# Kernel optimization log

Hardware: AMD Instinct MI355X
Metric: run time of the kernel (lower is better)

## Reference

```python
import jax, jax.numpy as jnp
import numpy as np

D_MODEL, H, D_K, D_V, D_FF = 1024, 16, 64, 64, 4096
B, L = 2, 2048
EPS = 1e-5


def layer_norm(x, g, b):
    mu = jnp.mean(x, axis=-1, keepdims=True)
    var = jnp.mean(jnp.square(x - mu), axis=-1, keepdims=True)
    return (x - mu) * jax.lax.rsqrt(var + EPS) * g + b


def setup_inputs() -> dict:
    key = jax.random.key(0)
    ks = jax.random.split(key, 12)
    s = 0.02
    x = jax.random.normal(ks[0], (B, L, D_MODEL), dtype=jnp.float32)
    Wq = jax.random.normal(ks[1], (H, D_MODEL, D_K), dtype=jnp.float32) * s
    Wk = jax.random.normal(ks[2], (H, D_MODEL, D_K), dtype=jnp.float32) * s
    Wv = jax.random.normal(ks[3], (H, D_MODEL, D_V), dtype=jnp.float32) * s
    bq = jnp.zeros((H, D_K), dtype=jnp.float32)
    bk = jnp.zeros((H, D_K), dtype=jnp.float32)
    bv = jnp.zeros((H, D_V), dtype=jnp.float32)
    Wo = jax.random.normal(ks[4], (H * D_V, D_MODEL), dtype=jnp.float32) * s
    W1 = jax.random.normal(ks[5], (D_MODEL, D_FF), dtype=jnp.float32) * s
    b1 = jnp.zeros((D_FF,), dtype=jnp.float32)
    W2 = jax.random.normal(ks[6], (D_FF, D_MODEL), dtype=jnp.float32) * s
    ln1_g = jnp.ones((D_MODEL,), dtype=jnp.float32)
    ln1_b = jnp.zeros((D_MODEL,), dtype=jnp.float32)
    ln2_g = jnp.ones((D_MODEL,), dtype=jnp.float32)
    ln2_b = jnp.zeros((D_MODEL,), dtype=jnp.float32)
    return dict(x=x, Wq=Wq, bq=bq, Wk=Wk, bk=bk, Wv=Wv, bv=bv, Wo=Wo,
                ln1_g=ln1_g, ln1_b=ln1_b, W1=W1, b1=b1, W2=W2,
                ln2_g=ln2_g, ln2_b=ln2_b)


def reference(x, Wq, bq, Wk, bk, Wv, bv, Wo, ln1_g, ln1_b, W1, b1, W2, ln2_g, ln2_b):
    # Batched multi-head attention (all heads at once, equivalent to the
    # per-head Python loop in the original module).
    Q = jnp.einsum('bld,hdk->bhlk', x, Wq) + bq[None, :, None, :]
    K = jnp.einsum('bld,hdk->bhlk', x, Wk) + bk[None, :, None, :]
    V = jnp.einsum('bld,hdv->bhlv', x, Wv) + bv[None, :, None, :]
    scores = jnp.einsum('bhlk,bhmk->bhlm', Q, K) * (1.0 / jnp.sqrt(jnp.float32(D_K)))
    attn = jax.nn.softmax(scores, axis=-1)
    O = jnp.einsum('bhlm,bhmv->bhlv', attn, V)        # [b,h,l,dv]
    O = jnp.transpose(O, (0, 2, 1, 3)).reshape(x.shape[0], x.shape[1], H * D_V)
    mha = O @ Wo                                       # [b,l,d_model]
    # residual + LayerNorm (dropout_prob=0 -> identity)
    h1 = layer_norm(x + mha, ln1_g, ln1_b)
    ff = jax.nn.relu(h1 @ W1 + b1) @ W2
    return layer_norm(h1 + ff, ln2_g, ln2_b)
```

## Files before the change

kernel.cpp:

```cpp
#include <hip/hip_runtime.h>

typedef unsigned short u16;
typedef unsigned int u32;
typedef short bf16x8 __attribute__((ext_vector_type(8)));
typedef float f32x4 __attribute__((ext_vector_type(4)));
typedef unsigned int u32x2 __attribute__((ext_vector_type(2)));
typedef unsigned int u32x4 __attribute__((ext_vector_type(4)));

#define D_MODEL 1024
#define NH 16
#define DK 64
#define DFF 4096
#define BATCH 2
#define SEQ 2048
#define BL (BATCH*SEQ)
#define NQKV 3072
#define Q_SCALE 0.18033688011f

__device__ __forceinline__ float bfraw2f(u16 u) {
    union { u32 i; float f; } c; c.i = ((u32)u) << 16; return c.f;
}
__device__ __forceinline__ u16 f2bfraw(float f) {
    union { float f; u32 i; } c; c.f = f;
    u32 i = c.i;
    u32 lsb = (i >> 16) & 1u;
    i += 0x7fffu + lsb;
    return (u16)(i >> 16);
}
__device__ __forceinline__ u32 fasu(float f) {
    union { float f; u32 i; } c; c.f = f; return c.i;
}
__device__ __forceinline__ u32 pack_bf2(float lo, float hi) {
    return __builtin_amdgcn_perm(fasu(hi) + 0x8000u, fasu(lo) + 0x8000u,
                                 0x07060302u);
}
__device__ __forceinline__ void gload_lds16(const u16* g, u16* l) {
    __builtin_amdgcn_global_load_lds(
        (const __attribute__((address_space(1))) void*)g,
        (__attribute__((address_space(3))) void*)l, 16, 0, 0);
}

__global__ __launch_bounds__(256) void cast_f32_bf16(const float* __restrict__ in,
                                                     u16* __restrict__ out) {
    int i = (blockIdx.x * 256 + threadIdx.x) * 4;
    f32x4 v = *(const f32x4*)&in[i];
#pragma unroll
    for (int j = 0; j < 4; j++) out[i + j] = f2bfraw(v[j]);
}


__global__ __launch_bounds__(256) void transpose2d(const float* __restrict__ in,
                                                   u16* __restrict__ out,
                                                   int R, int C) {
    __shared__ u16 t[64][65];
    int c0 = blockIdx.x * 64, r0 = blockIdx.y * 64;
    int col = threadIdx.x & 63, rr = threadIdx.x >> 6;
    for (int i = rr; i < 64; i += 4)
        t[i][col] = f2bfraw(in[(size_t)(r0 + i) * C + c0 + col]);
    __syncthreads();
    for (int i = rr; i < 64; i += 4)
        out[(size_t)(c0 + i) * R + r0 + col] = t[col][i];
}

__global__ __launch_bounds__(256) void transpose_wqkv(const float* __restrict__ Wq,
                                                      const float* __restrict__ Wk,
                                                      const float* __restrict__ Wv,
                                                      u16* __restrict__ out) {
    __shared__ u16 t[64][65];
    int d0 = blockIdx.x * 64;
    int h = blockIdx.y;
    int ms = blockIdx.z;
    const float* W = (ms == 0) ? Wq : (ms == 1) ? Wk : Wv;
    const float* src = W + (size_t)h * D_MODEL * DK;
    int col = threadIdx.x & 63, rr = threadIdx.x >> 6;
    for (int i = rr; i < 64; i += 4)
        t[i][col] = f2bfraw(src[(size_t)(d0 + i) * DK + col]);
    __syncthreads();
    u16* dst = out + (size_t)(ms * 1024 + h * 64) * D_MODEL;
    for (int i = rr; i < 64; i += 4)
        dst[(size_t)i * D_MODEL + d0 + col] = t[col][i];
}

__global__ __launch_bounds__(256) void concat_bias(const float* __restrict__ bq,
                                                   const float* __restrict__ bk,
                                                   const float* __restrict__ bv,
                                                   float* __restrict__ out) {
    int i = blockIdx.x * 256 + threadIdx.x;
    out[i] = (i < 1024) ? bq[i] : (i < 2048) ? bk[i - 1024] : bv[i - 2048];
}


template <int OUT_F32, int RELU, int HASBIAS, int SPLITK, int SCALEQ, int VSTORE>
__global__ __launch_bounds__(256, 4) void gemm_bt(const u16* __restrict__ A,
                                                  const u16* __restrict__ Bt,
                                                  const float* __restrict__ bias,
                                                  void* __restrict__ Cout,
                                                  u16* __restrict__ vtout,
                                                  int M, int N, int K) {
    __shared__ __attribute__((aligned(16))) u16 As[128 * 64];
    __shared__ __attribute__((aligned(16))) u16 Bs[128 * 64];
    const int tid = threadIdx.x;
    const int lane = tid & 63, wid = tid >> 6;
    const int quad = lane >> 4, l16 = lane & 15;
    const int m0 = blockIdx.x * 128, n0 = blockIdx.y * 128;
    const int z = (SPLITK > 1) ? blockIdx.z : 0;
    const int Klen = K / SPLITK;
    const int kend = (z + 1) * Klen;
    const int wm = (wid >> 1) * 64, wn = (wid & 1) * 64;

    f32x4 acc[4][4];
#pragma unroll
    for (int i = 0; i < 4; i++)
#pragma unroll
        for (int j = 0; j < 4; j++) acc[i][j] = (f32x4){0.f, 0.f, 0.f, 0.f};

    const int srow = lane >> 3, scol = (lane & 7) * 8;

    for (int kb = z * Klen; kb < kend; kb += 64) {
#pragma unroll
        for (int p = 0; p < 4; p++) {
            int c = wid * 4 + p;
            int row = c * 8 + srow;
            gload_lds16(&A[(size_t)(m0 + row) * K + kb + scol], &As[c * 512]);
            gload_lds16(&Bt[(size_t)(n0 + row) * K + kb + scol], &Bs[c * 512]);
        }
        __syncthreads();
#pragma unroll
        for (int kh = 0; kh < 2; kh++) {
            bf16x8 af[4], bf[4];
#pragma unroll
            for (int t = 0; t < 4; t++) {
                af[t] = *(const bf16x8*)&As[(wm + t * 16 + l16) * 64 + kh * 32 + quad * 8];
                bf[t] = *(const bf16x8*)&Bs[(wn + t * 16 + l16) * 64 + kh * 32 + quad * 8];
            }
#pragma unroll
            for (int i = 0; i < 4; i++)
#pragma unroll
                for (int j = 0; j < 4; j++)
                    acc[i][j] = __builtin_amdgcn_mfma_f32_16x16x32_bf16(
                        af[i], bf[j], acc[i][j], 0, 0, 0);
        }
        __syncthreads();
    }

    if (VSTORE && n0 >= 2048) {
#pragma unroll
        for (int i = 0; i < 4; i++) {
            int row0 = m0 + wm + i * 16 + quad * 4;
            int bb = row0 >> 11, l = row0 & 2047;
#pragma unroll
            for (int j = 0; j < 4; j++) {
                int col = n0 + wn + j * 16 + l16;
                float bv = HASBIAS ? bias[col] : 0.f;
                int dv = col - 2048;
                u32x2 w;
                w.x = pack_bf2(acc[i][j][0] + bv, acc[i][j][1] + bv);
                w.y = pack_bf2(acc[i][j][2] + bv, acc[i][j][3] + bv);
                *(u32x2*)&vtout[((size_t)(bb * 1024 + dv)) * 2048 + l] = w;
            }
        }
        return;
    }

    float* outf = (float*)Cout + (size_t)z * M * N;
#pragma unroll
    for (int i = 0; i < 4; i++) {
#pragma unroll
        for (int j = 0; j < 4; j++) {
#pragma unroll
            for (int r = 0; r < 4; r++) {
                int row = m0 + wm + i * 16 + quad * 4 + r;
                int col = n0 + wn + j * 16 + l16;
                float v = acc[i][j][r];
                if (HASBIAS) v += bias[col];
                if (RELU) v = v > 0.f ? v : 0.f;
                if (SCALEQ && col < 1024) v *= Q_SCALE;
                if (OUT_F32)
                    outf[(size_t)row * N + col] = v;
                else
                    ((u16*)Cout)[(size_t)row * N + col] = f2bfraw(v);
            }
        }
    }
}

__global__ __launch_bounds__(512, 4) void attn_kernel(const u16* __restrict__ qkv,
                                                      const u16* __restrict__ vt,
                                                      u16* __restrict__ O) {
    __shared__ __attribute__((aligned(16))) u16 Ks[2][128 * 64];
    __shared__ __attribute__((aligned(16))) u16 Vs[64 * 128];

    const int tid = threadIdx.x;
    const int lane = tid & 63, wid = tid >> 6;
    const int quad = lane >> 4, l16 = lane & 15;
    const int sw = l16 & 7;
    const int b = blockIdx.z, h = blockIdx.y;
    const int q0 = blockIdx.x * 128 + wid * 16;

    const size_t qrow = (size_t)(b * SEQ + q0 + l16) * NQKV + h * DK;
    const bf16x8 qf0 = *(const bf16x8*)&qkv[qrow + quad * 8];
    const bf16x8 qf1 = *(const bf16x8*)&qkv[qrow + 32 + quad * 8];

    const u16* Kbase = qkv + (size_t)(b * SEQ) * NQKV + D_MODEL + h * DK;
    const u16* Vbase = vt + (size_t)((b * NH + h) * DK) * SEQ;

    f32x4 oacc[4];
#pragma unroll
    for (int d = 0; d < 4; d++) oacc[d] = (f32x4){0.f, 0.f, 0.f, 0.f};
    float lr = 0.f;
    const f32x4 Z = {0.f, 0.f, 0.f, 0.f};

    auto stage_k = [&](int kt2, int buf) {
#pragma unroll
        for (int p = 0; p < 2; p++) {
            int seg = p * 8 + wid;
            int row = seg * 8 + (lane >> 3);
            int chunk = (lane & 7) ^ (lane >> 3);
            gload_lds16(&Kbase[(size_t)(kt2 + row) * NQKV + chunk * 8],
                        &Ks[buf][seg * 512]);
        }
    };
    bf16x8 vreg[2];
    auto load_v = [&](int kt2) {
#pragma unroll
        for (int p = 0; p < 2; p++) {
            int s = p * 512 + tid;
            vreg[p] = *(const bf16x8*)&Vbase[(size_t)(s >> 4) * SEQ + kt2 + (s & 15) * 8];
        }
    };
    stage_k(0, 0);
    load_v(0);

    for (int t = 0; t < SEQ / 128; t++) {
        const int kt = t * 128;
#pragma unroll
        for (int p = 0; p < 2; p++) {
            int s = p * 512 + tid;
            int vr = s >> 4, vc = s & 15;
            int chunkA = (vc >> 2) * 4 + (vc & 1) * 2;
            int rem = ((vc >> 1) & 1) * 4;
            u32x4 kv = __builtin_bit_cast(u32x4, vreg[p]);
            *(u32x2*)&Vs[vr * 128 + ((chunkA ^ (vr & 7)) * 8) + rem] =
                (u32x2){kv.x, kv.y};
            *(u32x2*)&Vs[vr * 128 + (((chunkA + 1) ^ (vr & 7)) * 8) + rem] =
                (u32x2){kv.z, kv.w};
        }
        __syncthreads();

        if (t + 1 < SEQ / 128) {
            stage_k(kt + 128, (t + 1) & 1);
            load_v(kt + 128);
        }

        const u16* kb = Ks[t & 1];

        f32x4 sacc[8];
        __builtin_amdgcn_s_setprio(1);
#pragma unroll
        for (int nt = 0; nt < 8; nt++) {
            const u16* krow = &kb[(nt * 16 + l16) * 64];
            bf16x8 kf0 = *(const bf16x8*)&krow[(quad ^ sw) * 8];
            bf16x8 kf1 = *(const bf16x8*)&krow[((4 + quad) ^ sw) * 8];
            f32x4 s0 = __builtin_amdgcn_mfma_f32_16x16x32_bf16(kf0, qf0, Z, 0, 0, 0);
            sacc[nt] = __builtin_amdgcn_mfma_f32_16x16x32_bf16(kf1, qf1, s0, 0, 0, 0);
        }
        __builtin_amdgcn_s_setprio(0);

        u32 wreg[8][2];
#pragma unroll
        for (int nt = 0; nt < 8; nt++) {
            float p0 = __builtin_amdgcn_exp2f(sacc[nt][0]);
            float p1 = __builtin_amdgcn_exp2f(sacc[nt][1]);
            float p2 = __builtin_amdgcn_exp2f(sacc[nt][2]);
            float p3 = __builtin_amdgcn_exp2f(sacc[nt][3]);
            lr += (p0 + p1) + (p2 + p3);
            wreg[nt][0] = pack_bf2(p0, p1);
            wreg[nt][1] = pack_bf2(p2, p3);
        }

        __builtin_amdgcn_s_setprio(1);
#pragma unroll
        for (int ks = 0; ks < 4; ks++) {
            u32x4 pw = (u32x4){wreg[2 * ks][0], wreg[2 * ks][1],
                               wreg[2 * ks + 1][0], wreg[2 * ks + 1][1]};
            bf16x8 pf = __builtin_bit_cast(bf16x8, pw);
#pragma unroll
            for (int d = 0; d < 4; d++) {
                bf16x8 vf = *(const bf16x8*)&Vs[(d * 16 + l16) * 128 +
                                                (((ks * 4 + quad) ^ sw) * 8)];
                oacc[d] = __builtin_amdgcn_mfma_f32_16x16x32_bf16(vf, pf, oacc[d], 0, 0, 0);
            }
        }
        __builtin_amdgcn_s_setprio(0);
        __syncthreads();
    }

    lr += __shfl_xor(lr, 16, 64);
    lr += __shfl_xor(lr, 32, 64);
    float iv = 1.f / lr;

    size_t row = (size_t)(b * SEQ + q0 + l16);
#pragma unroll
    for (int d = 0; d < 4; d++) {
        float o0 = oacc[d][0] * iv, o1 = oacc[d][1] * iv;
        float o2 = oacc[d][2] * iv, o3 = oacc[d][3] * iv;
        u32x2 w;
        w.x = ((u32)f2bfraw(o1) << 16) | f2bfraw(o0);
        w.y = ((u32)f2bfraw(o3) << 16) | f2bfraw(o2);
        *(u32x2*)&O[row * D_MODEL + h * DK + d * 16 + quad * 4] = w;
    }
}

__global__ __launch_bounds__(256) void ln3_kernel(const float* __restrict__ xa,
                                                  const float* __restrict__ xb,
                                                  const float* __restrict__ xc,
                                                  const float* __restrict__ g,
                                                  const float* __restrict__ be,
                                                  u16* __restrict__ out_bf,
                                                  float* __restrict__ out_f) {
    int row = blockIdx.x;
    int tid = threadIdx.x;
    const float* pa = xa + (size_t)row * D_MODEL;
    const float* pb = xb + (size_t)row * D_MODEL;
    const float* pc = xc + (size_t)row * D_MODEL;
    int c = tid * 4;
    f32x4 av = *(const f32x4*)&pa[c];
    f32x4 bv = *(const f32x4*)&pb[c];
    f32x4 cv = *(const f32x4*)&pc[c];
    float v[4];
    float s = 0.f, ss = 0.f;
#pragma unroll
    for (int i = 0; i < 4; i++) {
        v[i] = av[i] + bv[i] + cv[i];
        s += v[i];
        ss += v[i] * v[i];
    }
#pragma unroll
    for (int off = 32; off; off >>= 1) {
        s += __shfl_down(s, off, 64);
        ss += __shfl_down(ss, off, 64);
    }
    __shared__ float red[8];
    int wid = tid >> 6, lane = tid & 63;
    if (lane == 0) { red[wid] = s; red[4 + wid] = ss; }
    __syncthreads();
    if (tid == 0) {
        red[0] = red[0] + red[1] + red[2] + red[3];
        red[4] = red[4] + red[5] + red[6] + red[7];
    }
    __syncthreads();
    float mu = red[0] * (1.f / D_MODEL);
    float var = red[4] * (1.f / D_MODEL) - mu * mu;
    float rs = rsqrtf(var + 1e-5f);
#pragma unroll
    for (int i = 0; i < 4; i++) {
        float o = (v[i] - mu) * rs * g[c + i] + be[c + i];
        if (out_f) out_f[(size_t)row * D_MODEL + c + i] = o;
        if (out_bf) out_bf[(size_t)row * D_MODEL + c + i] = f2bfraw(o);
    }
}

extern "C" void kernel_launch(void* const* d_in, const int* in_sizes, int n_in,
                              void* d_out, int out_size, void* d_ws, size_t ws_size,
                              hipStream_t stream) {
    const float* x   = (const float*)d_in[0];
    const float* Wq  = (const float*)d_in[1];
    const float* bq  = (const float*)d_in[2];
    const float* Wk  = (const float*)d_in[3];
    const float* bk  = (const float*)d_in[4];
    const float* Wv  = (const float*)d_in[5];
    const float* bv  = (const float*)d_in[6];
    const float* Wo  = (const float*)d_in[7];
    const float* g1  = (const float*)d_in[8];
    const float* be1 = (const float*)d_in[9];
    const float* W1  = (const float*)d_in[10];
    const float* b1  = (const float*)d_in[11];
    const float* W2  = (const float*)d_in[12];
    const float* g2  = (const float*)d_in[13];
    const float* be2 = (const float*)d_in[14];

    char* w = (char*)d_ws;
    auto alloc = [&](size_t bytes) {
        char* p = w;
        w += (bytes + 255) & ~(size_t)255;
        return p;
    };
    u16* wqkv_t = (u16*)alloc((size_t)NQKV * D_MODEL * 2);
    u16* wo_t   = (u16*)alloc((size_t)D_MODEL * D_MODEL * 2);
    u16* w1_t   = (u16*)alloc((size_t)DFF * D_MODEL * 2);
    u16* w2_t   = (u16*)alloc((size_t)D_MODEL * DFF * 2);
    float* bqkv = (float*)alloc((size_t)NQKV * 4);
    u16* x_bf   = (u16*)alloc((size_t)BL * D_MODEL * 2);
    u16* qkvbuf = (u16*)alloc((size_t)BL * NQKV * 2);
    u16* vtbuf  = (u16*)alloc((size_t)BATCH * NH * DK * SEQ * 2);
    u16* obuf   = (u16*)alloc((size_t)BL * D_MODEL * 2);
    float* mha_p = (float*)alloc((size_t)2 * BL * D_MODEL * 4);
    u16* h1_bf  = (u16*)alloc((size_t)BL * D_MODEL * 2);
    float* h1_f = (float*)alloc((size_t)BL * D_MODEL * 4);
    u16* ffa    = (u16*)alloc((size_t)BL * DFF * 2);
    float* ffb_p = (float*)alloc((size_t)2 * BL * D_MODEL * 4);

    cast_f32_bf16<<<dim3(BL * D_MODEL / 1024), 256, 0, stream>>>(x, x_bf);
    transpose_wqkv<<<dim3(16, 16, 3), 256, 0, stream>>>(Wq, Wk, Wv, wqkv_t);
    transpose2d<<<dim3(16, 16), 256, 0, stream>>>(Wo, wo_t, 1024, 1024);
    transpose2d<<<dim3(64, 16), 256, 0, stream>>>(W1, w1_t, 1024, 4096);
    transpose2d<<<dim3(16, 64), 256, 0, stream>>>(W2, w2_t, 4096, 1024);
    concat_bias<<<dim3(12), 256, 0, stream>>>(bq, bk, bv, bqkv);

    gemm_bt<0, 0, 1, 1, 1, 1><<<dim3(32, 24), 256, 0, stream>>>(
        x_bf, wqkv_t, bqkv, qkvbuf, vtbuf, BL, NQKV, D_MODEL);
    attn_kernel<<<dim3(16, 16, 2), 512, 0, stream>>>(qkvbuf, vtbuf, obuf);
    gemm_bt<1, 0, 0, 2, 0, 0><<<dim3(32, 8, 2), 256, 0, stream>>>(
        obuf, wo_t, nullptr, mha_p, nullptr, BL, D_MODEL, D_MODEL);
    ln3_kernel<<<dim3(BL), 256, 0, stream>>>(x, mha_p, mha_p + (size_t)BL * D_MODEL,
                                             g1, be1, h1_bf, h1_f);
    gemm_bt<0, 1, 1, 1, 0, 0><<<dim3(32, 32), 256, 0, stream>>>(
        h1_bf, w1_t, b1, ffa, nullptr, BL, DFF, D_MODEL);
    gemm_bt<1, 0, 0, 2, 0, 0><<<dim3(32, 8, 2), 256, 0, stream>>>(
        ffa, w2_t, nullptr, ffb_p, nullptr, BL, D_MODEL, DFF);
    ln3_kernel<<<dim3(BL), 256, 0, stream>>>(h1_f, ffb_p, ffb_p + (size_t)BL * D_MODEL,
                                             g2, be2, nullptr, (float*)d_out);
}
```

Baseline: 369.7 us.

## Replace GEMM with larger-tile double-buffered swizzled kernel

Replaces the 128x128 GEMM with a 512-thread kernel using 256-wide N tiles (BM 256 or 128). It double-buffers LDS loads so the next K tile is fetched while the current one computes, and XOR-swizzles LDS layout to avoid bank conflicts. It also remaps workgroup order across XCDs and raises wave priority around MFMA. Larger tiles cut global traffic per FLOP but reduce block count, which may underfill CUs for some GEMMs.

```diff
diff --git a/kernel.cpp b/kernel.cpp
--- a/kernel.cpp
+++ b/kernel.cpp
@@ -90,67 +90,99 @@
 }
 
 
-template <int OUT_F32, int RELU, int HASBIAS, int SPLITK, int SCALEQ, int VSTORE>
-__global__ __launch_bounds__(256, 4) void gemm_bt(const u16* __restrict__ A,
-                                                  const u16* __restrict__ Bt,
-                                                  const float* __restrict__ bias,
-                                                  void* __restrict__ Cout,
-                                                  u16* __restrict__ vtout,
-                                                  int M, int N, int K) {
-    __shared__ __attribute__((aligned(16))) u16 As[128 * 64];
-    __shared__ __attribute__((aligned(16))) u16 Bs[128 * 64];
+template <int BM, int OUT_F32, int RELU, int HASBIAS, int SPLITK, int SCALEQ, int VSTORE>
+__global__ __launch_bounds__(512, 2) void gemm2(const u16* __restrict__ A,
+                                                const u16* __restrict__ Bt,
+                                                const float* __restrict__ bias,
+                                                void* __restrict__ Cout,
+                                                u16* __restrict__ vtout,
+                                                int M, int N, int K) {
+    constexpr int MF = BM / 32;
+    __shared__ __attribute__((aligned(16))) u16 As[2][BM * 64];
+    __shared__ __attribute__((aligned(16))) u16 Bs[2][256 * 64];
     const int tid = threadIdx.x;
     const int lane = tid & 63, wid = tid >> 6;
     const int quad = lane >> 4, l16 = lane & 15;
-    const int m0 = blockIdx.x * 128, n0 = blockIdx.y * 128;
+
+    int nwg = gridDim.x * gridDim.y;
+    int flat = blockIdx.y * gridDim.x + blockIdx.x;
+    if ((nwg & 7) == 0) {
+        int q = nwg >> 3;
+        flat = (flat & 7) * q + (flat >> 3);
+    }
+    const int m0 = (flat % gridDim.x) * BM;
+    const int n0 = (flat / gridDim.x) * 256;
+
     const int z = (SPLITK > 1) ? blockIdx.z : 0;
     const int Klen = K / SPLITK;
-    const int kend = (z + 1) * Klen;
-    const int wm = (wid >> 1) * 64, wn = (wid & 1) * 64;
-
-    f32x4 acc[4][4];
-#pragma unroll
-    for (int i = 0; i < 4; i++)
+    const int NT = Klen / 64;
+    const int kb0 = z * Klen;
+
+    const int wrow = (wid >> 2) * (BM / 2);
+    const int wcol = (wid & 3) * 64;
+
+    f32x4 acc[MF][4];
+#pragma unroll
+    for (int i = 0; i < MF; i++)
 #pragma unroll
         for (int j = 0; j < 4; j++) acc[i][j] = (f32x4){0.f, 0.f, 0.f, 0.f};
 
-    const int srow = lane >> 3, scol = (lane & 7) * 8;
-
-    for (int kb = z * Klen; kb < kend; kb += 64) {
+    auto stage = [&](int kb, int slot) {
+#pragma unroll
+        for (int p = 0; p < BM / 64; p++) {
+            int ew = p * 512 + wid * 64;
+            int e = ew + lane;
+            int row = e >> 3, ch = e & 7;
+            gload_lds16(&A[(size_t)(m0 + row) * K + kb + ((ch ^ (row & 7)) * 8)],
+                        &As[slot][ew * 8]);
+        }
 #pragma unroll
         for (int p = 0; p < 4; p++) {
-            int c = wid * 4 + p;
-            int row = c * 8 + srow;
-            gload_lds16(&A[(size_t)(m0 + row) * K + kb + scol], &As[c * 512]);
-            gload_lds16(&Bt[(size_t)(n0 + row) * K + kb + scol], &Bs[c * 512]);
-        }
+            int ew = p * 512 + wid * 64;
+            int e = ew + lane;
+            int row = e >> 3, ch = e & 7;
+            gload_lds16(&Bt[(size_t)(n0 + row) * K + kb + ((ch ^ (row & 7)) * 8)],
+                        &Bs[slot][ew * 8]);
+        }
+    };
+
+    stage(kb0, 0);
+    for (int t = 0; t < NT; t++) {
         __syncthreads();
-#pragma unroll
-        for (int kh = 0; kh < 2; kh++) {
-            bf16x8 af[4], bf[4];
-#pragma unroll
-            for (int t = 0; t < 4; t++) {
-                af[t] = *(const bf16x8*)&As[(wm + t * 16 + l16) * 64 + kh * 32 + quad * 8];
-                bf[t] = *(const bf16x8*)&Bs[(wn + t * 16 + l16) * 64 + kh * 32 + quad * 8];
+        if (t + 1 < NT) stage(kb0 + (t + 1) * 64, (t + 1) & 1);
+        const u16* as = As[t & 1];
+        const u16* bs = Bs[t & 1];
+        __builtin_amdgcn_s_setprio(1);
+        bf16x8 bfr[4][2];
+#pragma unroll
+        for (int j = 0; j < 4; j++) {
+            int rb = wcol + j * 16 + l16;
+#pragma unroll
+            for (int kh = 0; kh < 2; kh++)
+                bfr[j][kh] = *(const bf16x8*)&bs[rb * 64 + (((kh * 4 + quad) ^ (rb & 7)) * 8)];
+        }
+#pragma unroll
+        for (int i = 0; i < MF; i++) {
+            int ra = wrow + i * 16 + l16;
+            bf16x8 a0 = *(const bf16x8*)&as[ra * 64 + ((quad ^ (ra & 7)) * 8)];
+            bf16x8 a1 = *(const bf16x8*)&as[ra * 64 + (((4 + quad) ^ (ra & 7)) * 8)];
+#pragma unroll
+            for (int j = 0; j < 4; j++) {
+                acc[i][j] = __builtin_amdgcn_mfma_f32_16x16x32_bf16(a0, bfr[j][0], acc[i][j], 0, 0, 0);
+                acc[i][j] = __builtin_amdgcn_mfma_f32_16x16x32_bf16(a1, bfr[j][1], acc[i][j], 0, 0, 0);
             }
-#pragma unroll
-            for (int i = 0; i < 4; i++)
-#pragma unroll
-                for (int j = 0; j < 4; j++)
-                    acc[i][j] = __builtin_amdgcn_mfma_f32_16x16x32_bf16(
-                        af[i], bf[j], acc[i][j], 0, 0, 0);
-        }
-        __syncthreads();
+        }
+        __builtin_amdgcn_s_setprio(0);
     }
 
     if (VSTORE && n0 >= 2048) {
 #pragma unroll
-        for (int i = 0; i < 4; i++) {
-            int row0 = m0 + wm + i * 16 + quad * 4;
+        for (int i = 0; i < MF; i++) {
+            int row0 = m0 + wrow + i * 16 + quad * 4;
             int bb = row0 >> 11, l = row0 & 2047;
 #pragma unroll
             for (int j = 0; j < 4; j++) {
-                int col = n0 + wn + j * 16 + l16;
+                int col = n0 + wcol + j * 16 + l16;
                 float bv = HASBIAS ? bias[col] : 0.f;
                 int dv = col - 2048;
                 u32x2 w;
@@ -164,13 +196,13 @@
 
     float* outf = (float*)Cout + (size_t)z * M * N;
 #pragma unroll
-    for (int i = 0; i < 4; i++) {
+    for (int i = 0; i < MF; i++) {
 #pragma unroll
         for (int j = 0; j < 4; j++) {
 #pragma unroll
             for (int r = 0; r < 4; r++) {
-                int row = m0 + wm + i * 16 + quad * 4 + r;
-                int col = n0 + wn + j * 16 + l16;
+                int row = m0 + wrow + i * 16 + quad * 4 + r;
+                int col = n0 + wcol + j * 16 + l16;
                 float v = acc[i][j][r];
                 if (HASBIAS) v += bias[col];
                 if (RELU) v = v > 0.f ? v : 0.f;
@@ -407,16 +439,16 @@
     transpose2d<<<dim3(16, 64), 256, 0, stream>>>(W2, w2_t, 4096, 1024);
     concat_bias<<<dim3(12), 256, 0, stream>>>(bq, bk, bv, bqkv);
 
-    gemm_bt<0, 0, 1, 1, 1, 1><<<dim3(32, 24), 256, 0, stream>>>(
+    gemm2<256, 0, 0, 1, 1, 1, 1><<<dim3(16, 12), 512, 0, stream>>>(
         x_bf, wqkv_t, bqkv, qkvbuf, vtbuf, BL, NQKV, D_MODEL);
     attn_kernel<<<dim3(16, 16, 2), 512, 0, stream>>>(qkvbuf, vtbuf, obuf);
-    gemm_bt<1, 0, 0, 2, 0, 0><<<dim3(32, 8, 2), 256, 0, stream>>>(
+    gemm2<128, 1, 0, 0, 2, 0, 0><<<dim3(32, 4, 2), 512, 0, stream>>>(
         obuf, wo_t, nullptr, mha_p, nullptr, BL, D_MODEL, D_MODEL);
     ln3_kernel<<<dim3(BL), 256, 0, stream>>>(x, mha_p, mha_p + (size_t)BL * D_MODEL,
                                              g1, be1, h1_bf, h1_f);
-    gemm_bt<0, 1, 1, 1, 0, 0><<<dim3(32, 32), 256, 0, stream>>>(
+    gemm2<256, 0, 1, 1, 1, 0, 0><<<dim3(16, 16), 512, 0, stream>>>(
         h1_bf, w1_t, b1, ffa, nullptr, BL, DFF, D_MODEL);
-    gemm_bt<1, 0, 0, 2, 0, 0><<<dim3(32, 8, 2), 256, 0, stream>>>(
+    gemm2<128, 1, 0, 0, 2, 0, 0><<<dim3(32, 4, 2), 512, 0, stream>>>(
         ffa, w2_t, nullptr, ffb_p, nullptr, BL, D_MODEL, DFF);
     ln3_kernel<<<dim3(BL), 256, 0, stream>>>(h1_f, ffb_p, ffb_p + (size_t)BL * D_MODEL,
                                              g2, be2, nullptr, (float*)d_out);
```

Result: no change. 376.9 us (+2.0%).

## Add 256x256 pipelined GEMM kernel for QKV and FFN1 projections

Applied to the files above, without the earlier changes.

Introduces a new GEMM kernel with 256x256 tiles and 512 threads. It double-buffers swizzled LDS stages loaded directly from global memory, interleaves loads with MFMA phases under barriers and priority hints, and remaps workgroups for L2 locality. The kernel replaces the 128x128 gemm_bt for the QKV projection (with the V-transpose epilogue moved over) and for the first FFN GEMM. This aims to raise data reuse per tile and hide load latency. The trade-off is fewer workgroups (192 and 256) on a GPU with many CUs, plus more register pressure.

```diff
diff --git a/kernel.cpp b/kernel.cpp
--- a/kernel.cpp
+++ b/kernel.cpp
@@ -89,7 +89,6 @@
     out[i] = (i < 1024) ? bq[i] : (i < 2048) ? bk[i - 1024] : bv[i - 2048];
 }
 
-
 template <int OUT_F32, int RELU, int HASBIAS, int SPLITK, int SCALEQ, int VSTORE>
 __global__ __launch_bounds__(256, 4) void gemm_bt(const u16* __restrict__ A,
                                                   const u16* __restrict__ Bt,
@@ -143,25 +142,6 @@
         __syncthreads();
     }
 
-    if (VSTORE && n0 >= 2048) {
-#pragma unroll
-        for (int i = 0; i < 4; i++) {
-            int row0 = m0 + wm + i * 16 + quad * 4;
-            int bb = row0 >> 11, l = row0 & 2047;
-#pragma unroll
-            for (int j = 0; j < 4; j++) {
-                int col = n0 + wn + j * 16 + l16;
-                float bv = HASBIAS ? bias[col] : 0.f;
-                int dv = col - 2048;
-                u32x2 w;
-                w.x = pack_bf2(acc[i][j][0] + bv, acc[i][j][1] + bv);
-                w.y = pack_bf2(acc[i][j][2] + bv, acc[i][j][3] + bv);
-                *(u32x2*)&vtout[((size_t)(bb * 1024 + dv)) * 2048 + l] = w;
-            }
-        }
-        return;
-    }
-
     float* outf = (float*)Cout + (size_t)z * M * N;
 #pragma unroll
     for (int i = 0; i < 4; i++) {
@@ -171,6 +151,194 @@
             for (int r = 0; r < 4; r++) {
                 int row = m0 + wm + i * 16 + quad * 4 + r;
                 int col = n0 + wn + j * 16 + l16;
+                float v = acc[i][j][r];
+                if (HASBIAS) v += bias[col];
+                if (RELU) v = v > 0.f ? v : 0.f;
+                if (SCALEQ && col < 1024) v *= Q_SCALE;
+                if (OUT_F32)
+                    outf[(size_t)row * N + col] = v;
+                else
+                    ((u16*)Cout)[(size_t)row * N + col] = f2bfraw(v);
+            }
+        }
+    }
+}
+
+template <int OUT_F32, int RELU, int HASBIAS, int SCALEQ, int VSTORE>
+__global__ __launch_bounds__(512, 2) void gemm5(const u16* __restrict__ A,
+                                                const u16* __restrict__ Bt,
+                                                const float* __restrict__ bias,
+                                                void* __restrict__ Cout,
+                                                u16* __restrict__ vtout,
+                                                int M, int N, int K) {
+    __shared__ __attribute__((aligned(16))) u16 As[2][2][256 * 32];
+    __shared__ __attribute__((aligned(16))) u16 Bs[2][2][256 * 32];
+    const int tid = threadIdx.x;
+    const int lane = tid & 63, wid = tid >> 6;
+    const int quad = lane >> 4, l16 = lane & 15;
+
+    int nwg = gridDim.x * gridDim.y;
+    int flat = blockIdx.y * gridDim.x + blockIdx.x;
+    if ((nwg & 7) == 0) {
+        int q = nwg >> 3;
+        flat = (flat & 7) * q + (flat >> 3);
+    }
+    const int m0 = (flat % gridDim.x) * 256;
+    const int n0 = (flat / gridDim.x) * 256;
+
+    const int NTt = K >> 6;
+    const int wrow = (wid >> 2) * 128;
+    const int wcol = (wid & 3) * 64;
+
+    f32x4 acc[8][4];
+#pragma unroll
+    for (int i = 0; i < 8; i++)
+#pragma unroll
+        for (int j = 0; j < 4; j++) acc[i][j] = (f32x4){0.f, 0.f, 0.f, 0.f};
+
+    auto stageA = [&](int w, int kh) {
+        if (w >= NTt) return;
+        u16* dst = As[w & 1][kh];
+#pragma unroll
+        for (int p = 0; p < 2; p++) {
+            int e = p * 512 + tid;
+            int row = e >> 2, ch = e & 3;
+            gload_lds16(&A[(size_t)(m0 + row) * K + (w << 6) + (kh << 5) +
+                           (((ch ^ (row & 3))) << 3)],
+                        &dst[e * 8]);
+        }
+    };
+    auto stageB = [&](int w, int kh) {
+        if (w >= NTt) return;
+        u16* dst = Bs[w & 1][kh];
+#pragma unroll
+        for (int p = 0; p < 2; p++) {
+            int e = p * 512 + tid;
+            int row = e >> 2, ch = e & 3;
+            gload_lds16(&Bt[(size_t)(n0 + row) * K + (w << 6) + (kh << 5) +
+                            (((ch ^ (row & 3))) << 3)],
+                        &dst[e * 8]);
+        }
+    };
+
+    stageA(0, 0); stageB(0, 0);
+    stageA(0, 1); stageB(0, 1);
+    stageA(1, 0); stageB(1, 0);
+    asm volatile("s_waitcnt vmcnt(4)" ::: "memory");
+    __builtin_amdgcn_s_barrier();
+
+    for (int w = 0; w < NTt; w++) {
+        const u16* as0 = As[w & 1][0];
+        const u16* as1 = As[w & 1][1];
+        const u16* bs0 = Bs[w & 1][0];
+        const u16* bs1 = Bs[w & 1][1];
+        bf16x8 af[8], bf0, bf1;
+
+#pragma unroll
+        for (int i = 0; i < 8; i++) {
+            int ra = wrow + i * 16 + l16;
+            af[i] = *(const bf16x8*)&as0[ra * 32 + ((quad ^ (ra & 3)) * 8)];
+        }
+        {
+            int rb0 = wcol + l16, rb1 = wcol + 16 + l16;
+            bf0 = *(const bf16x8*)&bs0[rb0 * 32 + ((quad ^ (rb0 & 3)) * 8)];
+            bf1 = *(const bf16x8*)&bs0[rb1 * 32 + ((quad ^ (rb1 & 3)) * 8)];
+        }
+        stageA(w + 1, 1);
+        __builtin_amdgcn_s_barrier();
+        __builtin_amdgcn_s_setprio(1);
+#pragma unroll
+        for (int i = 0; i < 8; i++) {
+            acc[i][0] = __builtin_amdgcn_mfma_f32_16x16x32_bf16(af[i], bf0, acc[i][0], 0, 0, 0);
+            acc[i][1] = __builtin_amdgcn_mfma_f32_16x16x32_bf16(af[i], bf1, acc[i][1], 0, 0, 0);
+        }
+        __builtin_amdgcn_s_setprio(0);
+        __builtin_amdgcn_s_barrier();
+
+        {
+            int rb2 = wcol + 32 + l16, rb3 = wcol + 48 + l16;
+            bf0 = *(const bf16x8*)&bs0[rb2 * 32 + ((quad ^ (rb2 & 3)) * 8)];
+            bf1 = *(const bf16x8*)&bs0[rb3 * 32 + ((quad ^ (rb3 & 3)) * 8)];
+        }
+        stageB(w + 1, 1);
+        __builtin_amdgcn_s_barrier();
+        __builtin_amdgcn_s_setprio(1);
+#pragma unroll
+        for (int i = 0; i < 8; i++) {
+            acc[i][2] = __builtin_amdgcn_mfma_f32_16x16x32_bf16(af[i], bf0, acc[i][2], 0, 0, 0);
+            acc[i][3] = __builtin_amdgcn_mfma_f32_16x16x32_bf16(af[i], bf1, acc[i][3], 0, 0, 0);
+        }
+        __builtin_amdgcn_s_setprio(0);
+        __builtin_amdgcn_s_barrier();
+
+#pragma unroll
+        for (int i = 0; i < 8; i++) {
+            int ra = wrow + i * 16 + l16;
+            af[i] = *(const bf16x8*)&as1[ra * 32 + ((quad ^ (ra & 3)) * 8)];
+        }
+        {
+            int rb0 = wcol + l16, rb1 = wcol + 16 + l16;
+            bf0 = *(const bf16x8*)&bs1[rb0 * 32 + ((quad ^ (rb0 & 3)) * 8)];
+            bf1 = *(const bf16x8*)&bs1[rb1 * 32 + ((quad ^ (rb1 & 3)) * 8)];
+        }
+        stageA(w + 2, 0);
+        __builtin_amdgcn_s_barrier();
+        __builtin_amdgcn_s_setprio(1);
+#pragma unroll
+        for (int i = 0; i < 8; i++) {
+            acc[i][0] = __builtin_amdgcn_mfma_f32_16x16x32_bf16(af[i], bf0, acc[i][0], 0, 0, 0);
+            acc[i][1] = __builtin_amdgcn_mfma_f32_16x16x32_bf16(af[i], bf1, acc[i][1], 0, 0, 0);
+        }
+        __builtin_amdgcn_s_setprio(0);
+        __builtin_amdgcn_s_barrier();
+
+        {
+            int rb2 = wcol + 32 + l16, rb3 = wcol + 48 + l16;
+            bf0 = *(const bf16x8*)&bs1[rb2 * 32 + ((quad ^ (rb2 & 3)) * 8)];
+            bf1 = *(const bf16x8*)&bs1[rb3 * 32 + ((quad ^ (rb3 & 3)) * 8)];
+        }
+        stageB(w + 2, 0);
+        __builtin_amdgcn_s_barrier();
+        __builtin_amdgcn_s_setprio(1);
+#pragma unroll
+        for (int i = 0; i < 8; i++) {
+            acc[i][2] = __builtin_amdgcn_mfma_f32_16x16x32_bf16(af[i], bf0, acc[i][2], 0, 0, 0);
+            acc[i][3] = __builtin_amdgcn_mfma_f32_16x16x32_bf16(af[i], bf1, acc[i][3], 0, 0, 0);
+        }
+        __builtin_amdgcn_s_setprio(0);
+        if (w + 2 < NTt) asm volatile("s_waitcnt vmcnt(4)" ::: "memory");
+        else             asm volatile("s_waitcnt vmcnt(0)" ::: "memory");
+        __builtin_amdgcn_s_barrier();
+    }
+
+    if (VSTORE && n0 >= 2048) {
+#pragma unroll
+        for (int i = 0; i < 8; i++) {
+            int row0 = m0 + wrow + i * 16 + quad * 4;
+            int bb = row0 >> 11, l = row0 & 2047;
+#pragma unroll
+            for (int j = 0; j < 4; j++) {
+                int col = n0 + wcol + j * 16 + l16;
+                float bv = HASBIAS ? bias[col] : 0.f;
+                int dv = col - 2048;
+                u32x2 w2;
+                w2.x = pack_bf2(acc[i][j][0] + bv, acc[i][j][1] + bv);
+                w2.y = pack_bf2(acc[i][j][2] + bv, acc[i][j][3] + bv);
+                *(u32x2*)&vtout[((size_t)(bb * 1024 + dv)) * 2048 + l] = w2;
+            }
+        }
+        return;
+    }
+
+    float* outf = (float*)Cout;
+#pragma unroll
+    for (int i = 0; i < 8; i++) {
+#pragma unroll
+        for (int j = 0; j < 4; j++) {
+#pragma unroll
+            for (int r = 0; r < 4; r++) {
+                int row = m0 + wrow + i * 16 + quad * 4 + r;
+                int col = n0 + wcol + j * 16 + l16;
                 float v = acc[i][j][r];
                 if (HASBIAS) v += bias[col];
                 if (RELU) v = v > 0.f ? v : 0.f;
@@ -407,14 +575,14 @@
     transpose2d<<<dim3(16, 64), 256, 0, stream>>>(W2, w2_t, 4096, 1024);
     concat_bias<<<dim3(12), 256, 0, stream>>>(bq, bk, bv, bqkv);
 
-    gemm_bt<0, 0, 1, 1, 1, 1><<<dim3(32, 24), 256, 0, stream>>>(
+    gemm5<0, 0, 1, 1, 1><<<dim3(16, 12), 512, 0, stream>>>(
         x_bf, wqkv_t, bqkv, qkvbuf, vtbuf, BL, NQKV, D_MODEL);
     attn_kernel<<<dim3(16, 16, 2), 512, 0, stream>>>(qkvbuf, vtbuf, obuf);
     gemm_bt<1, 0, 0, 2, 0, 0><<<dim3(32, 8, 2), 256, 0, stream>>>(
         obuf, wo_t, nullptr, mha_p, nullptr, BL, D_MODEL, D_MODEL);
     ln3_kernel<<<dim3(BL), 256, 0, stream>>>(x, mha_p, mha_p + (size_t)BL * D_MODEL,
                                              g1, be1, h1_bf, h1_f);
-    gemm_bt<0, 1, 1, 1, 0, 0><<<dim3(32, 32), 256, 0, stream>>>(
+    gemm5<0, 1, 1, 0, 0><<<dim3(16, 16), 512, 0, stream>>>(
         h1_bf, w1_t, b1, ffa, nullptr, BL, DFF, D_MODEL);
     gemm_bt<1, 0, 0, 2, 0, 0><<<dim3(32, 8, 2), 256, 0, stream>>>(
         ffa, w2_t, nullptr, ffb_p, nullptr, BL, D_MODEL, DFF);
```

Result: no change. 376.0 us (+1.7%).
